# Optimization experiments

Measured on AMD Instinct MI355X. Metric: run time of the kernel, lower is better.

The kernel has to match this reference:

```python
import jax, jax.numpy as jnp
import numpy as np

D_MODEL = 1024
N_HEADS = 16
HEAD_DIM = D_MODEL // N_HEADS


def setup_inputs() -> dict:
    key = jax.random.key(0)
    ks = jax.random.split(key, 12)
    B, L = 2, 2048
    s = 1.0 / np.sqrt(D_MODEL)
    inp = {
        "q": jax.random.normal(ks[0], (B, L, D_MODEL), dtype=jnp.float32),
        "k": jax.random.normal(ks[1], (B, L, D_MODEL), dtype=jnp.float32),
        "v": jax.random.normal(ks[2], (B, L, D_MODEL), dtype=jnp.float32),
        "mask": jax.random.randint(ks[3], (B, L), 0, 2).astype(jnp.bool_),
        "Wq": jax.random.normal(ks[4], (D_MODEL, D_MODEL), dtype=jnp.float32) * s,
        "bq": jnp.zeros((D_MODEL,), dtype=jnp.float32),
        "Wk": jax.random.normal(ks[5], (D_MODEL, D_MODEL), dtype=jnp.float32) * s,
        "bk": jnp.zeros((D_MODEL,), dtype=jnp.float32),
        "Wv": jax.random.normal(ks[6], (D_MODEL, D_MODEL), dtype=jnp.float32) * s,
        "bv": jnp.zeros((D_MODEL,), dtype=jnp.float32),
        "Wo": jax.random.normal(ks[7], (D_MODEL, D_MODEL), dtype=jnp.float32) * s,
        "bo": jnp.zeros((D_MODEL,), dtype=jnp.float32),
    }
    return inp


def reference(q, k, v, mask, Wq, bq, Wk, bk, Wv, bv, Wo, bo):
    B, Lq, _ = q.shape
    Lk = k.shape[1]
    # torch Linear: y = x @ W.T + b; W is [out, in]
    Q = (jnp.einsum("bld,ed->ble", q, Wq) + bq).reshape(B, Lq, N_HEADS, HEAD_DIM).transpose(0, 2, 1, 3)
    K = (jnp.einsum("bld,ed->ble", k, Wk) + bk).reshape(B, Lk, N_HEADS, HEAD_DIM).transpose(0, 2, 1, 3)
    V = (jnp.einsum("bld,ed->ble", v, Wv) + bv).reshape(B, Lk, N_HEADS, HEAD_DIM).transpose(0, 2, 1, 3)
    scale = 1.0 / np.sqrt(HEAD_DIM).astype(np.float32)
    scores = jnp.einsum("bhqd,bhkd->bhqk", Q, K) * scale  # [B,H,Lq,Lk]
    # mask: True = masked out; broadcast (B,1,1,Lk)
    scores = jnp.where(mask[:, None, None, :], -jnp.inf, scores)
    attn = jax.nn.softmax(scores, axis=-1)
    out = jnp.einsum("bhqk,bhkd->bhqd", attn, V)  # [B,H,Lq,hd]
    out = out.transpose(0, 2, 1, 3).reshape(B, Lq, D_MODEL)
    return jnp.einsum("bld,ed->ble", out, Wo) + bo
```

## Files before the change

### kernel.cpp

```cpp
#include <hip/hip_runtime.h>

typedef unsigned short u16;
typedef __bf16 bf16x8 __attribute__((ext_vector_type(8)));
typedef float f32x4 __attribute__((ext_vector_type(4)));
typedef unsigned int u32x4 __attribute__((ext_vector_type(4)));
typedef unsigned int u32x2 __attribute__((ext_vector_type(2)));

#define MFMA16(a, b, c) __builtin_amdgcn_mfma_f32_16x16x32_bf16((a), (b), (c), 0, 0, 0)

__device__ __forceinline__ u16 f2bf(float f) {
    unsigned u = __builtin_bit_cast(unsigned, f);
    u = u + 0x7FFFu + ((u >> 16) & 1u);
    return (u16)(u >> 16);
}
__device__ __forceinline__ unsigned pk2(float a, float b) {
    return (unsigned)f2bf(a) | ((unsigned)f2bf(b) << 16);
}
__device__ __forceinline__ u32x4 pk8(f32x4 a, f32x4 b) {
    u32x4 r;
    r[0] = pk2(a[0], a[1]); r[1] = pk2(a[2], a[3]);
    r[2] = pk2(b[0], b[1]); r[3] = pk2(b[2], b[3]);
    return r;
}
__device__ __forceinline__ unsigned pkhu(float a, float b) {
    unsigned ua = __builtin_bit_cast(unsigned, a) + 0x8000u;
    unsigned ub = __builtin_bit_cast(unsigned, b) + 0x8000u;
    return __builtin_amdgcn_perm(ub, ua, 0x07060302u);
}
__device__ __forceinline__ float exp2_fast(float x) {
    float r;
    asm("v_exp_f32 %0, %1" : "=v"(r) : "v"(x));
    return r;
}
__device__ __forceinline__ void lds_load16(const u16* g, u16* l) {
    __builtin_amdgcn_global_load_lds(
        (const __attribute__((address_space(1))) void*)g,
        (__attribute__((address_space(3))) void*)l, 16, 0, 0);
}

#define QSCALE 0.18033688011112042f
#define FIXMAX 13.0f

__global__ __launch_bounds__(256) void convert_bf16(
    const float* __restrict__ q, const float* __restrict__ k, const float* __restrict__ v,
    const float* __restrict__ Wq, const float* __restrict__ Wk, const float* __restrict__ Wv,
    const float* __restrict__ Wo, u16* __restrict__ dst)
{
    const size_t i = ((size_t)blockIdx.x * 256 + threadIdx.x) * 8;
    const size_t QE = 4194304, WE = 1048576;
    const float* s;
    if (i < QE) s = q + i;
    else if (i < 2 * QE) s = k + (i - QE);
    else if (i < 3 * QE) s = v + (i - 2 * QE);
    else {
        size_t j = i - 3 * QE;
        if (j < WE) s = Wq + j;
        else if (j < 2 * WE) s = Wk + (j - WE);
        else if (j < 3 * WE) s = Wv + (j - 2 * WE);
        else s = Wo + (j - 3 * WE);
    }
    f32x4 a = *(const f32x4*)s;
    f32x4 b = *(const f32x4*)(s + 4);
    *(u32x4*)(dst + i) = pk8(a, b);
}

__device__ __forceinline__ void gemm128_core(
    const u16* __restrict__ A, const u16* __restrict__ B,
    int m0, int n0, u16* As, u16* Bs, int tid, f32x4 acc[4][4])
{
    const int wv = tid >> 6, lane = tid & 63, quad = lane >> 4, l16 = lane & 15;
    const int mh = (wv >> 1) * 64, nh = (wv & 1) * 64;
    const int segA0 = wv * 128 + lane;
    const int segA1 = wv * 128 + 64 + lane;
    const int ra0 = segA0 >> 2, ca0 = (segA0 & 3) * 8;
    const int ra1 = segA1 >> 2, ca1 = (segA1 & 3) * 8;
    u16* ldsA0 = &As[(wv * 128) * 8];
    u16* ldsA1 = &As[(wv * 128 + 64) * 8];
    u16* ldsB0 = &Bs[(wv * 128) * 8];
    u16* ldsB1 = &Bs[(wv * 128 + 64) * 8];
    const u16* gA = A + (size_t)m0 * 1024;
    const u16* gB = B + (size_t)n0 * 1024;

    for (int t = 0; t < 32; t++) {
        const int k0 = t * 32;
        __syncthreads();
        lds_load16(gA + (size_t)ra0 * 1024 + k0 + ca0, ldsA0);
        lds_load16(gA + (size_t)ra1 * 1024 + k0 + ca1, ldsA1);
        lds_load16(gB + (size_t)ra0 * 1024 + k0 + ca0, ldsB0);
        lds_load16(gB + (size_t)ra1 * 1024 + k0 + ca1, ldsB1);
        __syncthreads();
        bf16x8 af[4], bfr[4];
        #pragma unroll
        for (int mi = 0; mi < 4; mi++)
            af[mi] = *(const bf16x8*)&As[(mh + mi * 16 + l16) * 32 + quad * 8];
        #pragma unroll
        for (int ni = 0; ni < 4; ni++)
            bfr[ni] = *(const bf16x8*)&Bs[(nh + ni * 16 + l16) * 32 + quad * 8];
        #pragma unroll
        for (int mi = 0; mi < 4; mi++)
            #pragma unroll
            for (int ni = 0; ni < 4; ni++)
                acc[mi][ni] = MFMA16(af[mi], bfr[ni], acc[mi][ni]);
    }
}

__global__ __launch_bounds__(256) void qkv_bf(
    const u16* __restrict__ qb, const u16* __restrict__ kb, const u16* __restrict__ vb,
    const u16* __restrict__ wq, const u16* __restrict__ wk, const u16* __restrict__ wvv,
    const float* __restrict__ bq, const float* __restrict__ bk, const float* __restrict__ bv,
    u16* __restrict__ Qh, u16* __restrict__ Kh, u16* __restrict__ Vt)
{
    __shared__ alignas(16) u16 As[128 * 32];
    __shared__ alignas(16) u16 Bs[128 * 32];
    const int z = blockIdx.z;
    const u16* A = (z == 0) ? qb : (z == 1) ? kb : vb;
    const u16* B = (z == 0) ? wq : (z == 1) ? wk : wvv;
    const float* bias = (z == 0) ? bq : (z == 1) ? bk : bv;
    const int tid = threadIdx.x;
    const int id = blockIdx.x + (blockIdx.y << 3);
    const int xd = id >> 5;
    const int yd = ((id & 7) << 2) | ((id >> 3) & 3);
    const int m0 = yd * 128, n0 = xd * 128;
    const int wv = tid >> 6, lane = tid & 63, quad = lane >> 4, l16 = lane & 15;
    const int mh = (wv >> 1) * 64, nh = (wv & 1) * 64;

    f32x4 acc[4][4];
    #pragma unroll
    for (int i = 0; i < 4; i++)
        #pragma unroll
        for (int j = 0; j < 4; j++) acc[i][j] = (f32x4){0.f, 0.f, 0.f, 0.f};

    gemm128_core(A, B, m0, n0, As, Bs, tid, acc);

    const float scl = (z == 0) ? QSCALE : 1.0f;
    u16* outp = (z == 0) ? Qh : (z == 1) ? Kh : Vt;
    #pragma unroll
    for (int ni = 0; ni < 4; ni++) {
        const int n = n0 + nh + ni * 16 + l16;
        const float bval = bias[n];
        const int h = n >> 6, d = n & 63;
        #pragma unroll
        for (int mi = 0; mi < 4; mi++) {
            const int mbase = m0 + mh + mi * 16 + quad * 4;
            #pragma unroll
            for (int r = 0; r < 4; r++) {
                const int m = mbase + r;
                const int bb = m >> 11, l = m & 2047;
                const float val = (acc[mi][ni][r] + bval) * scl;
                size_t idx;
                if (z < 2) idx = (((size_t)(bb * 16 + h) * 2048 + l) << 6) + d;
                else       idx = (((size_t)(bb * 16 + h) * 64 + d) << 11) + l;
                outp[idx] = f2bf(val);
            }
        }
    }
}

__global__ __launch_bounds__(256) void out_bf(
    const u16* __restrict__ Ob, const u16* __restrict__ wo,
    const float* __restrict__ bo, float* __restrict__ out)
{
    __shared__ alignas(16) u16 As[128 * 32];
    __shared__ alignas(16) u16 Bs[128 * 32];
    const int tid = threadIdx.x;
    const int id = blockIdx.x + (blockIdx.y << 3);
    const int xd = id >> 5;
    const int yd = ((id & 7) << 2) | ((id >> 3) & 3);
    const int m0 = yd * 128, n0 = xd * 128;
    const int wv = tid >> 6, lane = tid & 63, quad = lane >> 4, l16 = lane & 15;
    const int mh = (wv >> 1) * 64, nh = (wv & 1) * 64;

    f32x4 acc[4][4];
    #pragma unroll
    for (int i = 0; i < 4; i++)
        #pragma unroll
        for (int j = 0; j < 4; j++) acc[i][j] = (f32x4){0.f, 0.f, 0.f, 0.f};

    gemm128_core(Ob, wo, m0, n0, As, Bs, tid, acc);

    #pragma unroll
    for (int ni = 0; ni < 4; ni++) {
        const int n = n0 + nh + ni * 16 + l16;
        const float bval = bo[n];
        #pragma unroll
        for (int mi = 0; mi < 4; mi++) {
            const int mbase = m0 + mh + mi * 16 + quad * 4;
            #pragma unroll
            for (int r = 0; r < 4; r++)
                out[(size_t)(mbase + r) * 1024 + n] = acc[mi][ni][r] + bval;
        }
    }
}

__global__ __launch_bounds__(256) void attn6(
    const u16* __restrict__ Qh, const u16* __restrict__ Kh,
    const u16* __restrict__ Vt, const int* __restrict__ mask,
    u16* __restrict__ Ob)
{
    __shared__ alignas(16) u16 Ks[2][64 * 72];
    __shared__ alignas(16) u16 Vs[2][64 * 72];
    __shared__ alignas(16) u16 Ps[4][16 * 72];
    __shared__ alignas(16) float Ms[2][64];

    const int tid = threadIdx.x;
    const int blk = blockIdx.x;
    const int bh = blk & 31, qt = blk >> 5;
    const int b = bh >> 4, h = bh & 15;
    const int wv = tid >> 6, lane = tid & 63, quad = lane >> 4, l16 = lane & 15;

    const int qbase = qt * 128 + wv * 32;
    const u16* Qb = Qh + ((size_t)bh * 2048 + qbase) * 64;
    bf16x8 qf[2][2];
    #pragma unroll
    for (int sub = 0; sub < 2; sub++)
        #pragma unroll
        for (int hf = 0; hf < 2; hf++)
            qf[sub][hf] = *(const bf16x8*)(Qb + (sub * 16 + l16) * 64 + hf * 32 + quad * 8);

    const u16* Kb = Kh + (size_t)bh * 2048 * 64;
    const u16* Vb = Vt + (size_t)bh * 64 * 2048;
    const int* mb = mask + b * 2048;

    const int s0 = tid, s1 = tid + 256;
    const int r0 = s0 >> 3, c0 = (s0 & 7) * 8;
    const int r1 = s1 >> 3, c1 = (s1 & 7) * 8;
    const int rp0 = ((r0 >> 2) & 3) * 16 + (r0 >> 4) * 4 + (r0 & 3);
    const int rp1 = ((r1 >> 2) & 3) * 16 + (r1 >> 4) * 4 + (r1 & 3);

    u32x4 rk0 = *(const u32x4*)(Kb + r0 * 64 + c0);
    u32x4 rk1 = *(const u32x4*)(Kb + r1 * 64 + c1);
    u32x4 rv0 = *(const u32x4*)(Vb + (size_t)r0 * 2048 + c0);
    u32x4 rv1 = *(const u32x4*)(Vb + (size_t)r1 * 2048 + c1);
    float rm = (tid < 64) ? (mb[tid] ? -1e30f : -FIXMAX) : 0.f;

    f32x4 o[2][4];
    #pragma unroll
    for (int sub = 0; sub < 2; sub++)
        #pragma unroll
        for (int db = 0; db < 4; db++) o[sub][db] = (f32x4){0.f, 0.f, 0.f, 0.f};
    float Lrun[2] = {0.f, 0.f};

    for (int kc = 0; kc < 32; kc++) {
        const int bi = kc & 1;
        u16* KsB = Ks[bi];
        u16* VsB = Vs[bi];
        *(u32x4*)&KsB[rp0 * 72 + c0] = rk0;
        *(u32x4*)&KsB[rp1 * 72 + c1] = rk1;
        *(u32x4*)&VsB[r0 * 72 + c0] = rv0;
        *(u32x4*)&VsB[r1 * 72 + c1] = rv1;
        if (tid < 64) Ms[bi][tid] = rm;
        __syncthreads();

        if (kc < 31) {
            const int off = (kc + 1) * 64;
            rk0 = *(const u32x4*)(Kb + (size_t)(off + r0) * 64 + c0);
            rk1 = *(const u32x4*)(Kb + (size_t)(off + r1) * 64 + c1);
            rv0 = *(const u32x4*)(Vb + (size_t)r0 * 2048 + off + c0);
            rv1 = *(const u32x4*)(Vb + (size_t)r1 * 2048 + off + c1);
            rm = (tid < 64) ? (mb[off + tid] ? -1e30f : -FIXMAX) : 0.f;
        }

        f32x4 st[2][4];
        #pragma unroll
        for (int nb = 0; nb < 4; nb++) {
            const bf16x8 kf0 = *(const bf16x8*)&KsB[(nb * 16 + l16) * 72 + quad * 8];
            const bf16x8 kf1 = *(const bf16x8*)&KsB[(nb * 16 + l16) * 72 + 32 + quad * 8];
            #pragma unroll
            for (int sub = 0; sub < 2; sub++) {
                f32x4 z = (f32x4){0.f, 0.f, 0.f, 0.f};
                z = MFMA16(kf0, qf[sub][0], z);
                z = MFMA16(kf1, qf[sub][1], z);
                st[sub][nb] = z;
            }
        }
        f32x4 mneg[4];
        #pragma unroll
        for (int nb = 0; nb < 4; nb++)
            mneg[nb] = *(const f32x4*)&Ms[bi][quad * 16 + nb * 4];

        bf16x8 pf[2][2];
        #pragma unroll
        for (int sub = 0; sub < 2; sub++) {
            #pragma unroll
            for (int nb = 0; nb < 4; nb++) {
                st[sub][nb] += mneg[nb];
                #pragma unroll
                for (int r = 0; r < 4; r++) st[sub][nb][r] = exp2_fast(st[sub][nb][r]);
            }
            f32x4 s4 = (st[sub][0] + st[sub][1]) + (st[sub][2] + st[sub][3]);
            float sm = (s4[0] + s4[1]) + (s4[2] + s4[3]);
            sm += __shfl_xor(sm, 16, 64);
            sm += __shfl_xor(sm, 32, 64);
            Lrun[sub] += sm;

            u16* prow = &Ps[wv][l16 * 72];
            u32x4 w;
            w[0] = pkhu(st[sub][0][0], st[sub][0][1]);
            w[1] = pkhu(st[sub][0][2], st[sub][0][3]);
            w[2] = pkhu(st[sub][1][0], st[sub][1][1]);
            w[3] = pkhu(st[sub][1][2], st[sub][1][3]);
            *(u32x4*)&prow[quad * 16] = w;
            w[0] = pkhu(st[sub][2][0], st[sub][2][1]);
            w[1] = pkhu(st[sub][2][2], st[sub][2][3]);
            w[2] = pkhu(st[sub][3][0], st[sub][3][1]);
            w[3] = pkhu(st[sub][3][2], st[sub][3][3]);
            *(u32x4*)&prow[quad * 16 + 8] = w;

            asm volatile("s_waitcnt lgkmcnt(0)" ::: "memory");
            pf[sub][0] = *(const bf16x8*)&Ps[wv][l16 * 72 + quad * 8];
            pf[sub][1] = *(const bf16x8*)&Ps[wv][l16 * 72 + 32 + quad * 8];
            asm volatile("" ::: "memory");
        }

        #pragma unroll
        for (int db = 0; db < 4; db++) {
            const bf16x8 vf0 = *(const bf16x8*)&VsB[(db * 16 + l16) * 72 + quad * 8];
            const bf16x8 vf1 = *(const bf16x8*)&VsB[(db * 16 + l16) * 72 + 32 + quad * 8];
            #pragma unroll
            for (int sub = 0; sub < 2; sub++) {
                o[sub][db] = MFMA16(pf[sub][0], vf0, o[sub][db]);
                o[sub][db] = MFMA16(pf[sub][1], vf1, o[sub][db]);
            }
        }
        asm volatile("" ::: "memory");
    }

    #pragma unroll
    for (int sub = 0; sub < 2; sub++) {
        const float li = 1.0f / Lrun[sub];
        #pragma unroll
        for (int r = 0; r < 4; r++) {
            const float lr = __shfl(li, (lane & 48) | (quad * 4 + r), 64);
            const int qrow = qt * 128 + wv * 32 + sub * 16 + quad * 4 + r;
            #pragma unroll
            for (int db = 0; db < 4; db++)
                Ob[((size_t)(b * 2048 + qrow)) * 1024 + h * 64 + db * 16 + l16] =
                    f2bf(o[sub][db][r] * lr);
        }
    }
}

__global__ __launch_bounds__(256) void qkv_gemm(
    const float* __restrict__ q, const float* __restrict__ k, const float* __restrict__ v,
    const float* __restrict__ Wq, const float* __restrict__ Wk, const float* __restrict__ Wv,
    const float* __restrict__ bq, const float* __restrict__ bk, const float* __restrict__ bv,
    u16* __restrict__ Qh, u16* __restrict__ Kh, u16* __restrict__ Vt)
{
    __shared__ alignas(16) u16 As[128 * 40];
    __shared__ alignas(16) u16 Bs[128 * 40];
    const int z = blockIdx.z;
    const float* A    = (z == 0) ? q  : (z == 1) ? k  : v;
    const float* W    = (z == 0) ? Wq : (z == 1) ? Wk : Wv;
    const float* bias = (z == 0) ? bq : (z == 1) ? bk : bv;
    const int tid = threadIdx.x;
    const int m0 = blockIdx.y * 128, n0 = blockIdx.x * 128;
    const int row = tid >> 1, cseg = tid & 1;
    const float* ga = A + (size_t)(m0 + row) * 1024 + cseg * 16;
    const float* gb = W + (size_t)(n0 + row) * 1024 + cseg * 16;
    const int wv = tid >> 6, lane = tid & 63, quad = lane >> 4, l16 = lane & 15;
    const int mh = (wv >> 1) * 64, nh = (wv & 1) * 64;

    f32x4 acc[4][4];
    for (int i = 0; i < 4; i++)
        for (int j = 0; j < 4; j++) acc[i][j] = (f32x4){0.f, 0.f, 0.f, 0.f};

    f32x4 ra[4], rb[4];
    for (int i = 0; i < 4; i++) {
        ra[i] = *(const f32x4*)(ga + i * 4);
        rb[i] = *(const f32x4*)(gb + i * 4);
    }
    for (int t = 0; t < 32; t++) {
        __syncthreads();
        *(u32x4*)&As[row * 40 + cseg * 16]     = pk8(ra[0], ra[1]);
        *(u32x4*)&As[row * 40 + cseg * 16 + 8] = pk8(ra[2], ra[3]);
        *(u32x4*)&Bs[row * 40 + cseg * 16]     = pk8(rb[0], rb[1]);
        *(u32x4*)&Bs[row * 40 + cseg * 16 + 8] = pk8(rb[2], rb[3]);
        __syncthreads();
        if (t < 31) {
            const int k0 = (t + 1) * 32;
            for (int i = 0; i < 4; i++) {
                ra[i] = *(const f32x4*)(ga + k0 + i * 4);
                rb[i] = *(const f32x4*)(gb + k0 + i * 4);
            }
        }
        bf16x8 af[4], bfr[4];
        for (int mi = 0; mi < 4; mi++)
            af[mi] = *(const bf16x8*)&As[(mh + mi * 16 + l16) * 40 + quad * 8];
        for (int ni = 0; ni < 4; ni++)
            bfr[ni] = *(const bf16x8*)&Bs[(nh + ni * 16 + l16) * 40 + quad * 8];
        for (int mi = 0; mi < 4; mi++)
            for (int ni = 0; ni < 4; ni++)
                acc[mi][ni] = MFMA16(af[mi], bfr[ni], acc[mi][ni]);
    }
    const float scl = (z == 0) ? QSCALE : 1.0f;
    u16* outp = (z == 0) ? Qh : (z == 1) ? Kh : Vt;
    for (int ni = 0; ni < 4; ni++) {
        const int n = n0 + nh + ni * 16 + l16;
        const float bval = bias[n];
        const int h = n >> 6, d = n & 63;
        for (int mi = 0; mi < 4; mi++) {
            const int mbase = m0 + mh + mi * 16 + quad * 4;
            for (int r = 0; r < 4; r++) {
                const int m = mbase + r;
                const int bb = m >> 11, l = m & 2047;
                const float val = (acc[mi][ni][r] + bval) * scl;
                size_t idx;
                if (z < 2) idx = (((size_t)(bb * 16 + h) * 2048 + l) << 6) + d;
                else       idx = (((size_t)(bb * 16 + h) * 64 + d) << 11) + l;
                outp[idx] = f2bf(val);
            }
        }
    }
}

__global__ __launch_bounds__(256) void out_gemm(
    const u16* __restrict__ Ob, const float* __restrict__ Wo,
    const float* __restrict__ bo, float* __restrict__ out)
{
    __shared__ alignas(16) u16 As[128 * 40];
    __shared__ alignas(16) u16 Bs[128 * 40];
    const int tid = threadIdx.x;
    const int m0 = blockIdx.y * 128, n0 = blockIdx.x * 128;
    const int row = tid >> 1, cseg = tid & 1;
    const u16* ga = Ob + (size_t)(m0 + row) * 1024 + cseg * 16;
    const float* gb = Wo + (size_t)(n0 + row) * 1024 + cseg * 16;
    const int wv = tid >> 6, lane = tid & 63, quad = lane >> 4, l16 = lane & 15;
    const int mh = (wv >> 1) * 64, nh = (wv & 1) * 64;

    f32x4 acc[4][4];
    for (int i = 0; i < 4; i++)
        for (int j = 0; j < 4; j++) acc[i][j] = (f32x4){0.f, 0.f, 0.f, 0.f};

    u32x4 ra0 = *(const u32x4*)(ga);
    u32x4 ra1 = *(const u32x4*)(ga + 8);
    f32x4 rb[4];
    for (int i = 0; i < 4; i++) rb[i] = *(const f32x4*)(gb + i * 4);

    for (int t = 0; t < 32; t++) {
        __syncthreads();
        *(u32x4*)&As[row * 40 + cseg * 16]     = ra0;
        *(u32x4*)&As[row * 40 + cseg * 16 + 8] = ra1;
        *(u32x4*)&Bs[row * 40 + cseg * 16]     = pk8(rb[0], rb[1]);
        *(u32x4*)&Bs[row * 40 + cseg * 16 + 8] = pk8(rb[2], rb[3]);
        __syncthreads();
        if (t < 31) {
            const int k0 = (t + 1) * 32;
            ra0 = *(const u32x4*)(ga + k0);
            ra1 = *(const u32x4*)(ga + k0 + 8);
            for (int i = 0; i < 4; i++) rb[i] = *(const f32x4*)(gb + k0 + i * 4);
        }
        bf16x8 af[4], bfr[4];
        for (int mi = 0; mi < 4; mi++)
            af[mi] = *(const bf16x8*)&As[(mh + mi * 16 + l16) * 40 + quad * 8];
        for (int ni = 0; ni < 4; ni++)
            bfr[ni] = *(const bf16x8*)&Bs[(nh + ni * 16 + l16) * 40 + quad * 8];
        for (int mi = 0; mi < 4; mi++)
            for (int ni = 0; ni < 4; ni++)
                acc[mi][ni] = MFMA16(af[mi], bfr[ni], acc[mi][ni]);
    }
    for (int ni = 0; ni < 4; ni++) {
        const int n = n0 + nh + ni * 16 + l16;
        const float bval = bo[n];
        for (int mi = 0; mi < 4; mi++) {
            const int mbase = m0 + mh + mi * 16 + quad * 4;
            for (int r = 0; r < 4; r++)
                out[(size_t)(mbase + r) * 1024 + n] = acc[mi][ni][r] + bval;
        }
    }
}

extern "C" void kernel_launch(void* const* d_in, const int* in_sizes, int n_in,
                              void* d_out, int out_size, void* d_ws, size_t ws_size,
                              hipStream_t stream)
{
    (void)in_sizes; (void)n_in; (void)out_size;
    const float* q  = (const float*)d_in[0];
    const float* k  = (const float*)d_in[1];
    const float* v  = (const float*)d_in[2];
    const int* mask = (const int*)d_in[3];
    const float* Wq = (const float*)d_in[4];
    const float* bq = (const float*)d_in[5];
    const float* Wk = (const float*)d_in[6];
    const float* bk = (const float*)d_in[7];
    const float* Wv = (const float*)d_in[8];
    const float* bv = (const float*)d_in[9];
    const float* Wo = (const float*)d_in[10];
    const float* bo = (const float*)d_in[11];
    float* out = (float*)d_out;

    u16* ws = (u16*)d_ws;
    const size_t QE = 4194304, WE = 1048576;
    const size_t NEED = (6 * QE + 4 * WE) * 2;

    if (ws_size >= NEED) {
        u16* qbf = ws;
        u16* kbf = ws + QE;
        u16* vbf = ws + 2 * QE;
        u16* wqb = ws + 3 * QE;
        u16* wkb = wqb + WE;
        u16* wvb = wqb + 2 * WE;
        u16* wob = wqb + 3 * WE;
        u16* Qh  = ws + 3 * QE + 4 * WE;
        u16* Kh  = Qh + QE;
        u16* Vth = Qh + 2 * QE;
        u16* Obp = qbf;
        convert_bf16<<<dim3(8192), 256, 0, stream>>>(q, k, v, Wq, Wk, Wv, Wo, ws);
        qkv_bf<<<dim3(8, 32, 3), 256, 0, stream>>>(qbf, kbf, vbf, wqb, wkb, wvb,
                                                   bq, bk, bv, Qh, Kh, Vth);
        attn6<<<dim3(512), 256, 0, stream>>>(Qh, Kh, Vth, mask, Obp);
        out_bf<<<dim3(8, 32), 256, 0, stream>>>(Obp, wob, bo, out);
    } else {
        u16* Qh  = ws;
        u16* Kh  = ws + QE;
        u16* Vth = ws + 2 * QE;
        u16* Obp = ws + 3 * QE;
        qkv_gemm<<<dim3(8, 32, 3), 256, 0, stream>>>(q, k, v, Wq, Wk, Wv,
                                                     bq, bk, bv, Qh, Kh, Vth);
        attn6<<<dim3(512), 256, 0, stream>>>(Qh, Kh, Vth, mask, Obp);
        out_gemm<<<dim3(8, 32), 256, 0, stream>>>(Obp, Wo, bo, out);
    }
}
```

Before: 236.9 us.

## Compute softmax row sums via MFMA with ones, use hardware bf16 pack, add setprio

```diff
diff --git a/kernel.cpp b/kernel.cpp
--- a/kernel.cpp
+++ b/kernel.cpp
@@ -22,10 +22,10 @@
     r[2] = pk2(b[0], b[1]); r[3] = pk2(b[2], b[3]);
     return r;
 }
-__device__ __forceinline__ unsigned pkhu(float a, float b) {
-    unsigned ua = __builtin_bit_cast(unsigned, a) + 0x8000u;
-    unsigned ub = __builtin_bit_cast(unsigned, b) + 0x8000u;
-    return __builtin_amdgcn_perm(ub, ua, 0x07060302u);
+__device__ __forceinline__ unsigned cvtpk(float a, float b) {
+    unsigned r;
+    asm("v_cvt_pk_bf16_f32 %0, %1, %2" : "=v"(r) : "v"(a), "v"(b));
+    return r;
 }
 __device__ __forceinline__ float exp2_fast(float x) {
     float r;
@@ -217,6 +217,9 @@
         for (int hf = 0; hf < 2; hf++)
             qf[sub][hf] = *(const bf16x8*)(Qb + (sub * 16 + l16) * 64 + hf * 32 + quad * 8);
 
+    const u32x4 onebits = {0x3F803F80u, 0x3F803F80u, 0x3F803F80u, 0x3F803F80u};
+    const bf16x8 onesf = __builtin_bit_cast(bf16x8, onebits);
+
     const u16* Kb = Kh + (size_t)bh * 2048 * 64;
     const u16* Vb = Vt + (size_t)bh * 64 * 2048;
     const int* mb = mask + b * 2048;
@@ -238,7 +241,9 @@
     for (int sub = 0; sub < 2; sub++)
         #pragma unroll
         for (int db = 0; db < 4; db++) o[sub][db] = (f32x4){0.f, 0.f, 0.f, 0.f};
-    float Lrun[2] = {0.f, 0.f};
+    f32x4 accL[2];
+    accL[0] = (f32x4){0.f, 0.f, 0.f, 0.f};
+    accL[1] = (f32x4){0.f, 0.f, 0.f, 0.f};
 
     for (int kc = 0; kc < 32; kc++) {
         const int bi = kc & 1;
@@ -261,6 +266,7 @@
         }
 
         f32x4 st[2][4];
+        __builtin_amdgcn_s_setprio(1);
         #pragma unroll
         for (int nb = 0; nb < 4; nb++) {
             const bf16x8 kf0 = *(const bf16x8*)&KsB[(nb * 16 + l16) * 72 + quad * 8];
@@ -273,6 +279,7 @@
                 st[sub][nb] = z;
             }
         }
+        __builtin_amdgcn_s_setprio(0);
         f32x4 mneg[4];
         #pragma unroll
         for (int nb = 0; nb < 4; nb++)
@@ -287,23 +294,18 @@
                 #pragma unroll
                 for (int r = 0; r < 4; r++) st[sub][nb][r] = exp2_fast(st[sub][nb][r]);
             }
-            f32x4 s4 = (st[sub][0] + st[sub][1]) + (st[sub][2] + st[sub][3]);
-            float sm = (s4[0] + s4[1]) + (s4[2] + s4[3]);
-            sm += __shfl_xor(sm, 16, 64);
-            sm += __shfl_xor(sm, 32, 64);
-            Lrun[sub] += sm;
 
             u16* prow = &Ps[wv][l16 * 72];
             u32x4 w;
-            w[0] = pkhu(st[sub][0][0], st[sub][0][1]);
-            w[1] = pkhu(st[sub][0][2], st[sub][0][3]);
-            w[2] = pkhu(st[sub][1][0], st[sub][1][1]);
-            w[3] = pkhu(st[sub][1][2], st[sub][1][3]);
+            w[0] = cvtpk(st[sub][0][0], st[sub][0][1]);
+            w[1] = cvtpk(st[sub][0][2], st[sub][0][3]);
+            w[2] = cvtpk(st[sub][1][0], st[sub][1][1]);
+            w[3] = cvtpk(st[sub][1][2], st[sub][1][3]);
             *(u32x4*)&prow[quad * 16] = w;
-            w[0] = pkhu(st[sub][2][0], st[sub][2][1]);
-            w[1] = pkhu(st[sub][2][2], st[sub][2][3]);
-            w[2] = pkhu(st[sub][3][0], st[sub][3][1]);
-            w[3] = pkhu(st[sub][3][2], st[sub][3][3]);
+            w[0] = cvtpk(st[sub][2][0], st[sub][2][1]);
+            w[1] = cvtpk(st[sub][2][2], st[sub][2][3]);
+            w[2] = cvtpk(st[sub][3][0], st[sub][3][1]);
+            w[3] = cvtpk(st[sub][3][2], st[sub][3][3]);
             *(u32x4*)&prow[quad * 16 + 8] = w;
 
             asm volatile("s_waitcnt lgkmcnt(0)" ::: "memory");
@@ -312,6 +314,7 @@
             asm volatile("" ::: "memory");
         }
 
+        __builtin_amdgcn_s_setprio(1);
         #pragma unroll
         for (int db = 0; db < 4; db++) {
             const bf16x8 vf0 = *(const bf16x8*)&VsB[(db * 16 + l16) * 72 + quad * 8];
@@ -322,15 +325,20 @@
                 o[sub][db] = MFMA16(pf[sub][1], vf1, o[sub][db]);
             }
         }
+        #pragma unroll
+        for (int sub = 0; sub < 2; sub++) {
+            accL[sub] = MFMA16(pf[sub][0], onesf, accL[sub]);
+            accL[sub] = MFMA16(pf[sub][1], onesf, accL[sub]);
+        }
+        __builtin_amdgcn_s_setprio(0);
         asm volatile("" ::: "memory");
     }
 
     #pragma unroll
     for (int sub = 0; sub < 2; sub++) {
-        const float li = 1.0f / Lrun[sub];
         #pragma unroll
         for (int r = 0; r < 4; r++) {
-            const float lr = __shfl(li, (lane & 48) | (quad * 4 + r), 64);
+            const float lr = __builtin_amdgcn_rcpf(accL[sub][r]);
             const int qrow = qt * 128 + wv * 32 + sub * 16 + quad * 4 + r;
             #pragma unroll
             for (int db = 0; db < 4; db++)
```

Result: faster. 229.3 us (-3.2%).
